# Kernel tuning notes

Measured on AMD Instinct MI355X. Metric: run time of the kernel, lower is better.

The kernel has to match this reference:

```python
import jax, jax.numpy as jnp
import numpy as np

B, S, E, H = 2, 2048, 1024, 16
D = E // H  # head_dim = 64


def setup_inputs() -> dict:
    key = jax.random.key(0)
    ks = jax.random.split(key, 6)
    scale = 1.0 / np.sqrt(E)
    x = jax.random.normal(ks[0], (B, S, E), dtype=jnp.float32)
    mask = jnp.ones((B, S), dtype=jnp.int32)
    Wqkv = jax.random.normal(ks[1], (E, 3 * E), dtype=jnp.float32) * scale
    bqkv = jax.random.normal(ks[2], (3 * E,), dtype=jnp.float32) * 0.01
    Wout = jax.random.normal(ks[3], (E, E), dtype=jnp.float32) * scale
    bout = jax.random.normal(ks[4], (E,), dtype=jnp.float32) * 0.01
    return {"x": x, "mask": mask, "Wqkv": Wqkv, "bqkv": bqkv, "Wout": Wout, "bout": bout}


def reference(x, mask, Wqkv, bqkv, Wout, bout):
    Bn, Sn, En = x.shape
    qkv = x @ Wqkv + bqkv                      # [B,S,3E]
    qkv = qkv.reshape(Bn, Sn, 3, H, D)
    qkv = jnp.transpose(qkv, (2, 0, 3, 1, 4))  # [3,B,H,S,D]
    q, k, v = qkv[0], qkv[1], qkv[2]
    scores = jnp.einsum('bhqd,bhkd->bhqk', q, k) / np.sqrt(D).astype(np.float32)
    m = mask[:, None, None, :]                 # [B,1,1,S]
    scores = jnp.where(m == 0, jnp.float32(-jnp.inf), scores)
    attn = jax.nn.softmax(scores, axis=-1)
    out = jnp.einsum('bhqk,bhkd->bhqd', attn, v)  # [B,H,S,D]
    out = jnp.transpose(out, (0, 2, 1, 3)).reshape(Bn, Sn, En)
    return out @ Wout + bout
```

## Files before the change

kernel.cpp:

```cpp
#include <hip/hip_runtime.h>


typedef __attribute__((ext_vector_type(8))) short short8;
typedef __attribute__((ext_vector_type(4))) float floatx4;
typedef unsigned short ushort_t;

static __device__ __forceinline__ ushort_t f2bf(float f) {
    unsigned u = __float_as_uint(f);
    u += 0x7fffu + ((u >> 16) & 1u);
    return (ushort_t)(u >> 16);
}
static __device__ __forceinline__ float bf2f(ushort_t h) {
    return __uint_as_float(((unsigned)h) << 16);
}
#if __has_builtin(__builtin_amdgcn_cvt_pk_bf16_f32)
typedef __attribute__((ext_vector_type(2))) __bf16 bf16x2_t;
static __device__ __forceinline__ unsigned pack2bf(float a, float b) {
    bf16x2_t r = __builtin_amdgcn_cvt_pk_bf16_f32(a, b);
    return __builtin_bit_cast(unsigned, r);
}
#else
static __device__ __forceinline__ unsigned pack2bf(float a, float b) {
    return (unsigned)f2bf(a) | ((unsigned)f2bf(b) << 16);
}
#endif
static __device__ __forceinline__ float hexp2(float x) {
    return __builtin_amdgcn_exp2f(x);
}
static __device__ __forceinline__ void gload16(const void* g, void* l) {
    __builtin_amdgcn_global_load_lds(
        (const __attribute__((address_space(1))) unsigned int*)g,
        (__attribute__((address_space(3))) unsigned int*)l, 16, 0, 0);
}

__global__ __launch_bounds__(256) void conv_hi(const float* __restrict__ in,
                                               ushort_t* __restrict__ out) {
    int i = blockIdx.x * 256 + threadIdx.x;
    float4 v = ((const float4*)in)[i];
    uint2 o;
    o.x = pack2bf(v.x, v.y);
    o.y = pack2bf(v.z, v.w);
    ((uint2*)out)[i] = o;
}

__global__ __launch_bounds__(256) void conv_T_hi(const float* __restrict__ W,
                                                 ushort_t* __restrict__ hiT,
                                                 int K, int N) {
    __shared__ float tile[32][33];
    const int nb = blockIdx.x * 32, kb = blockIdx.y * 32;
    const int t = threadIdx.x;
    const int r = t >> 3, c4 = (t & 7) * 4;
    float4 v = *(const float4*)&W[(size_t)(kb + r) * N + nb + c4];
    tile[r][c4 + 0] = v.x; tile[r][c4 + 1] = v.y;
    tile[r][c4 + 2] = v.z; tile[r][c4 + 3] = v.w;
    __syncthreads();
    uint2 o;
    o.x = pack2bf(tile[c4 + 0][r], tile[c4 + 1][r]);
    o.y = pack2bf(tile[c4 + 2][r], tile[c4 + 3][r]);
    size_t off = ((size_t)(nb + r) * K + kb + c4) >> 2;
    ((uint2*)hiT)[off] = o;
}

__global__ __launch_bounds__(256) void transpose_v(const ushort_t* __restrict__ qkvb,
                                                   ushort_t* __restrict__ vtg) {
    __shared__ ushort_t tile[64][72];
    const int b = blockIdx.z, h = blockIdx.y, s0 = blockIdx.x * 64;
    const int t = threadIdx.x;
    #pragma unroll
    for (int p = 0; p < 2; ++p) {
        int idx = t + p * 256;
        int sl = idx >> 3, dc = (idx & 7) * 8;
        *(uint4*)&tile[sl][dc] =
            *(const uint4*)&qkvb[(size_t)(b * 2048 + s0 + sl) * 3072 + 2048 + h * 64 + dc];
    }
    __syncthreads();
    #pragma unroll
    for (int p = 0; p < 2; ++p) {
        int idx = t + p * 256;
        int dl = idx >> 3, sc = (idx & 7) * 8;
        ushort_t v[8];
        #pragma unroll
        for (int j = 0; j < 8; ++j) v[j] = tile[sc + j][dl];
        *(uint4*)&vtg[(size_t)((b * 16 + h) * 64 + dl) * 2048 + s0 + sc] = *(const uint4*)v;
    }
}

__global__ __launch_bounds__(256, 3) void gemm_bf16_bf(
    const ushort_t* __restrict__ A, const ushort_t* __restrict__ B,
    const float* __restrict__ bias, ushort_t* __restrict__ C,
    int M, int N, int K)
{
    __shared__ ushort_t Ah[128][32], Bh[128][32];
    const int bn = blockIdx.x * 128, bm = blockIdx.y * 128;
    const int t = threadIdx.x, w = t >> 6, lane = t & 63;
    const int l15 = lane & 15, quad = lane >> 4;
    const int wm = w >> 1, wn = w & 1;

    const int srow = w * 32 + (lane >> 2);
    const int skp  = (lane & 3) ^ ((lane >> 2) & 3);
    const int scol = skp * 8;
    const ushort_t* ga = A + (size_t)(bm + srow) * K + scol;
    const ushort_t* gb = B + (size_t)(bn + srow) * K + scol;
    const size_t rstep = (size_t)16 * K;
    const int fcol = ((quad ^ (l15 & 3)) * 8);

    floatx4 acc[4][4];
    #pragma unroll
    for (int mt = 0; mt < 4; ++mt)
        #pragma unroll
        for (int nt = 0; nt < 4; ++nt) acc[mt][nt] = (floatx4){0.f, 0.f, 0.f, 0.f};

    for (int k0 = 0; k0 < K; k0 += 32) {
        #pragma unroll
        for (int i = 0; i < 2; ++i) {
            gload16(ga + i * rstep + k0, &Ah[w * 32 + i * 16][0]);
            gload16(gb + i * rstep + k0, &Bh[w * 32 + i * 16][0]);
        }
        __syncthreads();
        short8 ah[4], bh[4];
        #pragma unroll
        for (int x = 0; x < 4; ++x) {
            ah[x] = *(const short8*)&Ah[wm * 64 + x * 16 + l15][fcol];
            bh[x] = *(const short8*)&Bh[wn * 64 + x * 16 + l15][fcol];
        }
        #pragma unroll
        for (int mt = 0; mt < 4; ++mt)
            #pragma unroll
            for (int nt = 0; nt < 4; ++nt)
                acc[mt][nt] = __builtin_amdgcn_mfma_f32_16x16x32_bf16(ah[mt], bh[nt], acc[mt][nt], 0, 0, 0);
        __syncthreads();
    }
    #pragma unroll
    for (int mt = 0; mt < 4; ++mt)
        #pragma unroll
        for (int r = 0; r < 4; ++r) {
            size_t row = (size_t)(bm + wm * 64 + mt * 16 + quad * 4 + r) * N;
            #pragma unroll
            for (int nt = 0; nt < 4; ++nt) {
                int col = bn + wn * 64 + nt * 16 + l15;
                C[row + col] = f2bf(acc[mt][nt][r] + bias[col]);
            }
        }
}

__global__ __launch_bounds__(256, 3) void gemm_bf16_f32_64(
    const ushort_t* __restrict__ A, const ushort_t* __restrict__ B,
    const float* __restrict__ bias, float* __restrict__ C,
    int M, int N, int K)
{
    __shared__ ushort_t Ah[64][32], Bh[128][32];
    const int bn = blockIdx.x * 128, bm = blockIdx.y * 64;
    const int t = threadIdx.x, w = t >> 6, lane = t & 63;
    const int l15 = lane & 15, quad = lane >> 4;
    const int wm = w >> 1, wn = w & 1;

    const int srow = w * 16 + (lane >> 2);
    const int skp  = (lane & 3) ^ ((lane >> 2) & 3);
    const int scol = skp * 8;
    const ushort_t* ga  = A + (size_t)(bm + srow) * K + scol;
    const ushort_t* gb0 = B + (size_t)(bn + srow) * K + scol;
    const ushort_t* gb1 = B + (size_t)(bn + 64 + srow) * K + scol;
    const int fcol = ((quad ^ (l15 & 3)) * 8);

    floatx4 acc[2][4];
    #pragma unroll
    for (int mt = 0; mt < 2; ++mt)
        #pragma unroll
        for (int nt = 0; nt < 4; ++nt) acc[mt][nt] = (floatx4){0.f, 0.f, 0.f, 0.f};

    for (int k0 = 0; k0 < K; k0 += 32) {
        gload16(ga  + k0, &Ah[w * 16][0]);
        gload16(gb0 + k0, &Bh[w * 16][0]);
        gload16(gb1 + k0, &Bh[64 + w * 16][0]);
        __syncthreads();
        short8 ah[2], bh[4];
        #pragma unroll
        for (int x = 0; x < 2; ++x)
            ah[x] = *(const short8*)&Ah[wm * 32 + x * 16 + l15][fcol];
        #pragma unroll
        for (int x = 0; x < 4; ++x)
            bh[x] = *(const short8*)&Bh[wn * 64 + x * 16 + l15][fcol];
        #pragma unroll
        for (int mt = 0; mt < 2; ++mt)
            #pragma unroll
            for (int nt = 0; nt < 4; ++nt)
                acc[mt][nt] = __builtin_amdgcn_mfma_f32_16x16x32_bf16(ah[mt], bh[nt], acc[mt][nt], 0, 0, 0);
        __syncthreads();
    }
    #pragma unroll
    for (int mt = 0; mt < 2; ++mt)
        #pragma unroll
        for (int r = 0; r < 4; ++r) {
            size_t row = (size_t)(bm + wm * 32 + mt * 16 + quad * 4 + r) * N;
            #pragma unroll
            for (int nt = 0; nt < 4; ++nt) {
                int col = bn + wn * 64 + nt * 16 + l15;
                C[row + col] = acc[mt][nt][r] + bias[col];
            }
        }
}

__global__ __launch_bounds__(256, 3) void flash_v5(
    const ushort_t* __restrict__ qkv, const ushort_t* __restrict__ vtg,
    const int* __restrict__ mask,
    ushort_t* __restrict__ po0, ushort_t* __restrict__ po1,
    float* __restrict__ pl0, float* __restrict__ pl1, int S)
{
    __shared__ ushort_t Ks[64][64];
    __shared__ ushort_t Vt[64][64];
    __shared__ ushort_t Ps[4][16][72];
    __shared__ float Madd[64];

    const int blk = blockIdx.x;
    const int xcd = blk & 7, rr = blk >> 3;
    const int qi = rr & 15, g = xcd + 8 * (rr >> 4);
    const int half = g & 1, h = (g >> 1) & 15, b = g >> 5;
    const int q0 = qi * 128;
    const int kbase = half * 1024;

    ushort_t* po = half ? po1 : po0;
    float*    pl = half ? pl1 : pl0;

    const int t = threadIdx.x, wave = t >> 6, lane = t & 63;
    const int l15 = lane & 15, quad = lane >> 4;
    const size_t bS = (size_t)b * S;
    const float c1  = 0.125f * 1.44269504088896340736f;
    const float OFF = 24.0f;

    short8 qf[2][2];
    #pragma unroll
    for (int tt = 0; tt < 2; ++tt) {
        int q = q0 + wave * 32 + tt * 16 + l15;
        const ushort_t* qp = qkv + (bS + q) * 3072 + h * 64;
        qf[tt][0] = *(const short8*)(qp + quad * 8);
        qf[tt][1] = *(const short8*)(qp + 32 + quad * 8);
    }

    const int srow  = wave * 16 + (lane >> 3);
    const int schnk = ((lane & 7) ^ ((lane >> 3) & 7)) * 8;
    const ushort_t* gK = qkv + (bS + srow) * 3072 + 1024 + h * 64 + schnk;
    const ushort_t* gV = vtg + ((size_t)(b * 16 + h) * 64 + srow) * 2048 + schnk;

    floatx4 outacc[2][4];
    float lsum[2] = {0.f, 0.f};
    #pragma unroll
    for (int tt = 0; tt < 2; ++tt)
        #pragma unroll
        for (int dt = 0; dt < 4; ++dt) outacc[tt][dt] = (floatx4){0.f, 0.f, 0.f, 0.f};

    for (int k0 = kbase; k0 < kbase + 1024; k0 += 64) {
        gload16(gK + (size_t)k0 * 3072,             &Ks[wave * 16][0]);
        gload16(gK + (size_t)k0 * 3072 + 8 * 3072,  &Ks[wave * 16 + 8][0]);
        gload16(gV + k0,                            &Vt[wave * 16][0]);
        gload16(gV + k0 + 8 * 2048,                 &Vt[wave * 16 + 8][0]);
        if (t < 64) Madd[t] = (mask[bS + k0 + t] ? 0.f : -1e30f) - OFF;
        __syncthreads();

        short8 kf[2][4], vf[2][4];
        #pragma unroll
        for (int kc = 0; kc < 2; ++kc)
            #pragma unroll
            for (int c = 0; c < 4; ++c) {
                int ch = ((kc * 4 + quad) ^ (l15 & 7)) * 8;
                kf[kc][c] = *(const short8*)&Ks[c * 16 + l15][ch];
                vf[kc][c] = *(const short8*)&Vt[c * 16 + l15][ch];
            }
        float4 madd4[4];
        #pragma unroll
        for (int c = 0; c < 4; ++c) madd4[c] = *(const float4*)&Madd[c * 16 + quad * 4];

        #pragma unroll
        for (int tt = 0; tt < 2; ++tt) {
            floatx4 sc[4];
            #pragma unroll
            for (int c = 0; c < 4; ++c) {
                sc[c] = (floatx4){0.f, 0.f, 0.f, 0.f};
                sc[c] = __builtin_amdgcn_mfma_f32_16x16x32_bf16(kf[0][c], qf[tt][0], sc[c], 0, 0, 0);
                sc[c] = __builtin_amdgcn_mfma_f32_16x16x32_bf16(kf[1][c], qf[tt][1], sc[c], 0, 0, 0);
            }
            #pragma unroll
            for (int c = 0; c < 4; ++c) {
                float p0 = hexp2(fmaf(sc[c][0], c1, madd4[c].x));
                float p1 = hexp2(fmaf(sc[c][1], c1, madd4[c].y));
                float p2 = hexp2(fmaf(sc[c][2], c1, madd4[c].z));
                float p3 = hexp2(fmaf(sc[c][3], c1, madd4[c].w));
                lsum[tt] += (p0 + p1) + (p2 + p3);
                uint2 pk;
                pk.x = pack2bf(p0, p1);
                pk.y = pack2bf(p2, p3);
                *(uint2*)&Ps[wave][l15][c * 16 + quad * 4] = pk;
            }
            short8 pf0 = *(const short8*)&Ps[wave][l15][quad * 8];
            short8 pf1 = *(const short8*)&Ps[wave][l15][32 + quad * 8];
            #pragma unroll
            for (int dt = 0; dt < 4; ++dt) {
                outacc[tt][dt] = __builtin_amdgcn_mfma_f32_16x16x32_bf16(vf[0][dt], pf0, outacc[tt][dt], 0, 0, 0);
                outacc[tt][dt] = __builtin_amdgcn_mfma_f32_16x16x32_bf16(vf[1][dt], pf1, outacc[tt][dt], 0, 0, 0);
            }
        }
        __syncthreads();
    }

    #pragma unroll
    for (int tt = 0; tt < 2; ++tt) {
        lsum[tt] += __shfl_xor(lsum[tt], 16);
        lsum[tt] += __shfl_xor(lsum[tt], 32);
        lsum[tt] += 1e-30f;
        float inv = 1.f / lsum[tt];
        int q = q0 + wave * 32 + tt * 16 + l15;
        ushort_t* orow = po + (bS + q) * 1024 + h * 64;
        #pragma unroll
        for (int dt = 0; dt < 4; ++dt) {
            uint2 pk;
            pk.x = pack2bf(outacc[tt][dt][0] * inv, outacc[tt][dt][1] * inv);
            pk.y = pack2bf(outacc[tt][dt][2] * inv, outacc[tt][dt][3] * inv);
            *(uint2*)&orow[dt * 16 + quad * 4] = pk;
        }
        if (quad == 0) pl[(bS + q) * 16 + h] = lsum[tt];
    }
}

__global__ __launch_bounds__(256) void combine_halves(
    const ushort_t* __restrict__ po0, const ushort_t* __restrict__ po1,
    const float* __restrict__ pl0, const float* __restrict__ pl1,
    ushort_t* __restrict__ attnb)
{
    int i = blockIdx.x * 256 + threadIdx.x;
    int row = i >> 8;
    int h = (i >> 4) & 15;
    float l0 = pl0[row * 16 + h], l1 = pl1[row * 16 + h];
    float inv = 1.f / (l0 + l1);
    float w0 = l0 * inv, w1 = l1 * inv;
    uint2 a = ((const uint2*)po0)[i];
    uint2 b2 = ((const uint2*)po1)[i];
    float o0 = bf2f(a.x & 0xffff)  * w0 + bf2f(b2.x & 0xffff)  * w1;
    float o1 = bf2f(a.x >> 16)     * w0 + bf2f(b2.x >> 16)     * w1;
    float o2 = bf2f(a.y & 0xffff)  * w0 + bf2f(b2.y & 0xffff)  * w1;
    float o3 = bf2f(a.y >> 16)     * w0 + bf2f(b2.y >> 16)     * w1;
    uint2 o;
    o.x = pack2bf(o0, o1);
    o.y = pack2bf(o2, o3);
    ((uint2*)attnb)[i] = o;
}

extern "C" void kernel_launch(void* const* d_in, const int* in_sizes, int n_in,
                              void* d_out, int out_size, void* d_ws, size_t ws_size,
                              hipStream_t stream) {
    const float* x    = (const float*)d_in[0];
    const int*   mask = (const int*)  d_in[1];
    const float* Wqkv = (const float*)d_in[2];
    const float* bqkv = (const float*)d_in[3];
    const float* Wout = (const float*)d_in[4];
    const float* bout = (const float*)d_in[5];
    float* out = (float*)d_out;

    char* ws = (char*)d_ws;
    ushort_t* qkvb = (ushort_t*)(ws);
    ushort_t* attnb= (ushort_t*)(ws + 25165824);
    ushort_t* vtg  = (ushort_t*)(ws + 33554432);
    ushort_t* woT  = (ushort_t*)(ws + 41943040);
    ushort_t* xb   = (ushort_t*)(ws + 44040192);
    ushort_t* wqT  = (ushort_t*)(ws + 52428800);
    ushort_t* po0  = (ushort_t*)(ws + 44040192);
    ushort_t* po1  = (ushort_t*)(ws + 52428800);
    float*    pl0  = (float*)   (ws + 60817408);
    float*    pl1  = (float*)   (ws + 61079552);

    const int M = 4096, E = 1024, N3 = 3072, S = 2048;

    conv_hi<<<dim3(M * E / 1024), dim3(256), 0, stream>>>(x, xb);
    conv_T_hi<<<dim3(N3 / 32, E / 32), dim3(256), 0, stream>>>(Wqkv, wqT, E, N3);

    gemm_bf16_bf<<<dim3(N3 / 128, M / 128), dim3(256), 0, stream>>>(
        xb, wqT, bqkv, qkvb, M, N3, E);

    transpose_v<<<dim3(S / 64, 16, 2), dim3(256), 0, stream>>>(qkvb, vtg);

    flash_v5<<<dim3(1024), dim3(256), 0, stream>>>(
        qkvb, vtg, mask, po0, po1, pl0, pl1, S);

    combine_halves<<<dim3(M * E / 4 / 256), dim3(256), 0, stream>>>(
        po0, po1, pl0, pl1, attnb);

    conv_T_hi<<<dim3(E / 32, E / 32), dim3(256), 0, stream>>>(Wout, woT, E, E);

    gemm_bf16_f32_64<<<dim3(E / 128, M / 64), dim3(256), 0, stream>>>(
        attnb, woT, bout, out, M, E, E);
}
```

Before: 221.5 us.

## Fuse V transpose into QKV GEMM epilogue and drop split-K attention combine

The QKV GEMM epilogue now writes the V columns directly in transposed layout, so the separate transpose kernel is removed. Q and K are stored packed into a 2048-wide buffer. The flash kernel now processes the full key range per block (512 blocks instead of 1024), which eliminates the partial outputs and the combine_halves pass. It also double-buffers the K/V tiles in LDS, loads a precomputed additive mask once into LDS, and lowers occupancy to 2 blocks per CU. The trade-off is half as many attention blocks, a longer per-block loop, and more LDS per block.

New measurement: 208.2 us. 1.06x faster.

```diff
diff --git a/kernel.cpp b/kernel.cpp
--- a/kernel.cpp
+++ b/kernel.cpp
@@ -61,35 +61,18 @@
     ((uint2*)hiT)[off] = o;
 }
 
-__global__ __launch_bounds__(256) void transpose_v(const ushort_t* __restrict__ qkvb,
-                                                   ushort_t* __restrict__ vtg) {
-    __shared__ ushort_t tile[64][72];
-    const int b = blockIdx.z, h = blockIdx.y, s0 = blockIdx.x * 64;
-    const int t = threadIdx.x;
-    #pragma unroll
-    for (int p = 0; p < 2; ++p) {
-        int idx = t + p * 256;
-        int sl = idx >> 3, dc = (idx & 7) * 8;
-        *(uint4*)&tile[sl][dc] =
-            *(const uint4*)&qkvb[(size_t)(b * 2048 + s0 + sl) * 3072 + 2048 + h * 64 + dc];
-    }
-    __syncthreads();
-    #pragma unroll
-    for (int p = 0; p < 2; ++p) {
-        int idx = t + p * 256;
-        int dl = idx >> 3, sc = (idx & 7) * 8;
-        ushort_t v[8];
-        #pragma unroll
-        for (int j = 0; j < 8; ++j) v[j] = tile[sc + j][dl];
-        *(uint4*)&vtg[(size_t)((b * 16 + h) * 64 + dl) * 2048 + s0 + sc] = *(const uint4*)v;
-    }
-}
-
-__global__ __launch_bounds__(256, 3) void gemm_bf16_bf(
+__global__ __launch_bounds__(256) void conv_madd(const int* __restrict__ mask,
+                                                 float* __restrict__ maddg) {
+    int i = blockIdx.x * 256 + threadIdx.x;
+    maddg[i] = (mask[i] ? 0.f : -1e30f) - 24.0f;
+}
+
+__global__ __launch_bounds__(256, 3) void gemm_qkv(
     const ushort_t* __restrict__ A, const ushort_t* __restrict__ B,
-    const float* __restrict__ bias, ushort_t* __restrict__ C,
-    int M, int N, int K)
+    const float* __restrict__ bias, ushort_t* __restrict__ qkvb,
+    ushort_t* __restrict__ vtg)
 {
+    const int K = 1024;
     __shared__ ushort_t Ah[128][32], Bh[128][32];
     const int bn = blockIdx.x * 128, bm = blockIdx.y * 128;
     const int t = threadIdx.x, w = t >> 6, lane = t & 63;
@@ -130,17 +113,37 @@
                 acc[mt][nt] = __builtin_amdgcn_mfma_f32_16x16x32_bf16(ah[mt], bh[nt], acc[mt][nt], 0, 0, 0);
         __syncthreads();
     }
-    #pragma unroll
-    for (int mt = 0; mt < 4; ++mt)
-        #pragma unroll
-        for (int r = 0; r < 4; ++r) {
-            size_t row = (size_t)(bm + wm * 64 + mt * 16 + quad * 4 + r) * N;
+
+    if (bn < 2048) {
+        #pragma unroll
+        for (int mt = 0; mt < 4; ++mt)
+            #pragma unroll
+            for (int r = 0; r < 4; ++r) {
+                size_t row = (size_t)(bm + wm * 64 + mt * 16 + quad * 4 + r) * 2048;
+                #pragma unroll
+                for (int nt = 0; nt < 4; ++nt) {
+                    int col = bn + wn * 64 + nt * 16 + l15;
+                    qkvb[row + col] = f2bf(acc[mt][nt][r] + bias[col]);
+                }
+            }
+    } else {
+        const int h = (bn - 2048 + wn * 64) >> 6;
+        #pragma unroll
+        for (int mt = 0; mt < 4; ++mt) {
+            int brow = bm + wm * 64 + mt * 16 + quad * 4;
+            int b = brow >> 11, s = brow & 2047;
             #pragma unroll
             for (int nt = 0; nt < 4; ++nt) {
                 int col = bn + wn * 64 + nt * 16 + l15;
-                C[row + col] = f2bf(acc[mt][nt][r] + bias[col]);
-            }
-        }
+                int d = nt * 16 + l15;
+                float bv = bias[col];
+                uint2 pk;
+                pk.x = pack2bf(acc[mt][nt][0] + bv, acc[mt][nt][1] + bv);
+                pk.y = pack2bf(acc[mt][nt][2] + bv, acc[mt][nt][3] + bv);
+                *(uint2*)&vtg[((size_t)((b * 16 + h) * 64 + d)) * 2048 + s] = pk;
+            }
+        }
+    }
 }
 
 __global__ __launch_bounds__(256, 3) void gemm_bf16_f32_64(
@@ -200,46 +203,49 @@
         }
 }
 
-__global__ __launch_bounds__(256, 3) void flash_v5(
+__global__ __launch_bounds__(256, 2) void flash_v6(
     const ushort_t* __restrict__ qkv, const ushort_t* __restrict__ vtg,
-    const int* __restrict__ mask,
-    ushort_t* __restrict__ po0, ushort_t* __restrict__ po1,
-    float* __restrict__ pl0, float* __restrict__ pl1, int S)
+    const float* __restrict__ maddg, ushort_t* __restrict__ attn)
 {
-    __shared__ ushort_t Ks[64][64];
-    __shared__ ushort_t Vt[64][64];
-    __shared__ ushort_t Ps[4][16][72];
-    __shared__ float Madd[64];
+    __shared__ ushort_t Ks[2][64][64];
+    __shared__ ushort_t Vt[2][64][64];
+    __shared__ ushort_t Ps[4][2][16][72];
+    __shared__ float MaddL[2048];
 
     const int blk = blockIdx.x;
     const int xcd = blk & 7, rr = blk >> 3;
     const int qi = rr & 15, g = xcd + 8 * (rr >> 4);
-    const int half = g & 1, h = (g >> 1) & 15, b = g >> 5;
-    const int q0 = qi * 128;
-    const int kbase = half * 1024;
-
-    ushort_t* po = half ? po1 : po0;
-    float*    pl = half ? pl1 : pl0;
+    const int b = g >> 4, h = g & 15, q0 = qi * 128;
 
     const int t = threadIdx.x, wave = t >> 6, lane = t & 63;
     const int l15 = lane & 15, quad = lane >> 4;
-    const size_t bS = (size_t)b * S;
-    const float c1  = 0.125f * 1.44269504088896340736f;
-    const float OFF = 24.0f;
+    const size_t bS = (size_t)b * 2048;
+    const float c1 = 0.125f * 1.44269504088896340736f;
 
     short8 qf[2][2];
     #pragma unroll
     for (int tt = 0; tt < 2; ++tt) {
         int q = q0 + wave * 32 + tt * 16 + l15;
-        const ushort_t* qp = qkv + (bS + q) * 3072 + h * 64;
+        const ushort_t* qp = qkv + (bS + q) * 2048 + h * 64;
         qf[tt][0] = *(const short8*)(qp + quad * 8);
         qf[tt][1] = *(const short8*)(qp + 32 + quad * 8);
     }
 
     const int srow  = wave * 16 + (lane >> 3);
     const int schnk = ((lane & 7) ^ ((lane >> 3) & 7)) * 8;
-    const ushort_t* gK = qkv + (bS + srow) * 3072 + 1024 + h * 64 + schnk;
+    const ushort_t* gK = qkv + (bS + srow) * 2048 + 1024 + h * 64 + schnk;
     const ushort_t* gV = vtg + ((size_t)(b * 16 + h) * 64 + srow) * 2048 + schnk;
+
+    gload16(gK,            &Ks[0][wave * 16][0]);
+    gload16(gK + 8 * 2048, &Ks[0][wave * 16 + 8][0]);
+    gload16(gV,            &Vt[0][wave * 16][0]);
+    gload16(gV + 8 * 2048, &Vt[0][wave * 16 + 8][0]);
+    {
+        const float* gM = maddg + b * 2048 + wave * 512 + lane * 4;
+        gload16(gM,       &MaddL[wave * 512]);
+        gload16(gM + 256, &MaddL[wave * 512 + 256]);
+    }
+    __syncthreads();
 
     floatx4 outacc[2][4];
     float lsum[2] = {0.f, 0.f};
@@ -248,13 +254,17 @@
         #pragma unroll
         for (int dt = 0; dt < 4; ++dt) outacc[tt][dt] = (floatx4){0.f, 0.f, 0.f, 0.f};
 
-    for (int k0 = kbase; k0 < kbase + 1024; k0 += 64) {
-        gload16(gK + (size_t)k0 * 3072,             &Ks[wave * 16][0]);
-        gload16(gK + (size_t)k0 * 3072 + 8 * 3072,  &Ks[wave * 16 + 8][0]);
-        gload16(gV + k0,                            &Vt[wave * 16][0]);
-        gload16(gV + k0 + 8 * 2048,                 &Vt[wave * 16 + 8][0]);
-        if (t < 64) Madd[t] = (mask[bS + k0 + t] ? 0.f : -1e30f) - OFF;
-        __syncthreads();
+    int cur = 0;
+    for (int kt = 0; kt < 32; ++kt) {
+        const int k0 = kt * 64;
+        {
+            const int kn = (kt + 1 < 32) ? (kt + 1) * 64 : 0;
+            const int nb = cur ^ 1;
+            gload16(gK + (size_t)kn * 2048,            &Ks[nb][wave * 16][0]);
+            gload16(gK + (size_t)(kn + 8) * 2048,      &Ks[nb][wave * 16 + 8][0]);
+            gload16(gV + kn,                           &Vt[nb][wave * 16][0]);
+            gload16(gV + kn + 8 * 2048,                &Vt[nb][wave * 16 + 8][0]);
+        }
 
         short8 kf[2][4], vf[2][4];
         #pragma unroll
@@ -262,12 +272,13 @@
             #pragma unroll
             for (int c = 0; c < 4; ++c) {
                 int ch = ((kc * 4 + quad) ^ (l15 & 7)) * 8;
-                kf[kc][c] = *(const short8*)&Ks[c * 16 + l15][ch];
-                vf[kc][c] = *(const short8*)&Vt[c * 16 + l15][ch];
+                kf[kc][c] = *(const short8*)&Ks[cur][c * 16 + l15][ch];
+                vf[kc][c] = *(const short8*)&Vt[cur][c * 16 + l15][ch];
             }
         float4 madd4[4];
         #pragma unroll
-        for (int c = 0; c < 4; ++c) madd4[c] = *(const float4*)&Madd[c * 16 + quad * 4];
+        for (int c = 0; c < 4; ++c)
+            madd4[c] = *(const float4*)&MaddL[k0 + c * 16 + quad * 4];
 
         #pragma unroll
         for (int tt = 0; tt < 2; ++tt) {
@@ -288,10 +299,10 @@
                 uint2 pk;
                 pk.x = pack2bf(p0, p1);
                 pk.y = pack2bf(p2, p3);
-                *(uint2*)&Ps[wave][l15][c * 16 + quad * 4] = pk;
-            }
-            short8 pf0 = *(const short8*)&Ps[wave][l15][quad * 8];
-            short8 pf1 = *(const short8*)&Ps[wave][l15][32 + quad * 8];
+                *(uint2*)&Ps[wave][tt][l15][c * 16 + quad * 4] = pk;
+            }
+            short8 pf0 = *(const short8*)&Ps[wave][tt][l15][quad * 8];
+            short8 pf1 = *(const short8*)&Ps[wave][tt][l15][32 + quad * 8];
             #pragma unroll
             for (int dt = 0; dt < 4; ++dt) {
                 outacc[tt][dt] = __builtin_amdgcn_mfma_f32_16x16x32_bf16(vf[0][dt], pf0, outacc[tt][dt], 0, 0, 0);
@@ -299,16 +310,16 @@
             }
         }
         __syncthreads();
+        cur ^= 1;
     }
 
     #pragma unroll
     for (int tt = 0; tt < 2; ++tt) {
         lsum[tt] += __shfl_xor(lsum[tt], 16);
         lsum[tt] += __shfl_xor(lsum[tt], 32);
-        lsum[tt] += 1e-30f;
         float inv = 1.f / lsum[tt];
         int q = q0 + wave * 32 + tt * 16 + l15;
-        ushort_t* orow = po + (bS + q) * 1024 + h * 64;
+        ushort_t* orow = attn + (bS + q) * 1024 + h * 64;
         #pragma unroll
         for (int dt = 0; dt < 4; ++dt) {
             uint2 pk;
@@ -316,31 +327,7 @@
             pk.y = pack2bf(outacc[tt][dt][2] * inv, outacc[tt][dt][3] * inv);
             *(uint2*)&orow[dt * 16 + quad * 4] = pk;
         }
-        if (quad == 0) pl[(bS + q) * 16 + h] = lsum[tt];
-    }
-}
-
-__global__ __launch_bounds__(256) void combine_halves(
-    const ushort_t* __restrict__ po0, const ushort_t* __restrict__ po1,
-    const float* __restrict__ pl0, const float* __restrict__ pl1,
-    ushort_t* __restrict__ attnb)
-{
-    int i = blockIdx.x * 256 + threadIdx.x;
-    int row = i >> 8;
-    int h = (i >> 4) & 15;
-    float l0 = pl0[row * 16 + h], l1 = pl1[row * 16 + h];
-    float inv = 1.f / (l0 + l1);
-    float w0 = l0 * inv, w1 = l1 * inv;
-    uint2 a = ((const uint2*)po0)[i];
-    uint2 b2 = ((const uint2*)po1)[i];
-    float o0 = bf2f(a.x & 0xffff)  * w0 + bf2f(b2.x & 0xffff)  * w1;
-    float o1 = bf2f(a.x >> 16)     * w0 + bf2f(b2.x >> 16)     * w1;
-    float o2 = bf2f(a.y & 0xffff)  * w0 + bf2f(b2.y & 0xffff)  * w1;
-    float o3 = bf2f(a.y >> 16)     * w0 + bf2f(b2.y >> 16)     * w1;
-    uint2 o;
-    o.x = pack2bf(o0, o1);
-    o.y = pack2bf(o2, o3);
-    ((uint2*)attnb)[i] = o;
+    }
 }
 
 extern "C" void kernel_launch(void* const* d_in, const int* in_sizes, int n_in,
@@ -355,32 +342,24 @@
     float* out = (float*)d_out;
 
     char* ws = (char*)d_ws;
-    ushort_t* qkvb = (ushort_t*)(ws);
-    ushort_t* attnb= (ushort_t*)(ws + 25165824);
-    ushort_t* vtg  = (ushort_t*)(ws + 33554432);
-    ushort_t* woT  = (ushort_t*)(ws + 41943040);
-    ushort_t* xb   = (ushort_t*)(ws + 44040192);
-    ushort_t* wqT  = (ushort_t*)(ws + 52428800);
-    ushort_t* po0  = (ushort_t*)(ws + 44040192);
-    ushort_t* po1  = (ushort_t*)(ws + 52428800);
-    float*    pl0  = (float*)   (ws + 60817408);
-    float*    pl1  = (float*)   (ws + 61079552);
+    ushort_t* xb    = (ushort_t*)(ws);
+    ushort_t* wqT   = (ushort_t*)(ws + 8388608);
+    ushort_t* qkvb  = (ushort_t*)(ws + 14680064);
+    ushort_t* vtg   = (ushort_t*)(ws + 31457280);
+    ushort_t* attnb = (ushort_t*)(ws + 39845888);
+    ushort_t* woT   = (ushort_t*)(ws + 48234496);
+    float*    maddg = (float*)   (ws + 50331648);
 
     const int M = 4096, E = 1024, N3 = 3072, S = 2048;
 
     conv_hi<<<dim3(M * E / 1024), dim3(256), 0, stream>>>(x, xb);
     conv_T_hi<<<dim3(N3 / 32, E / 32), dim3(256), 0, stream>>>(Wqkv, wqT, E, N3);
-
-    gemm_bf16_bf<<<dim3(N3 / 128, M / 128), dim3(256), 0, stream>>>(
-        xb, wqT, bqkv, qkvb, M, N3, E);
-
-    transpose_v<<<dim3(S / 64, 16, 2), dim3(256), 0, stream>>>(qkvb, vtg);
-
-    flash_v5<<<dim3(1024), dim3(256), 0, stream>>>(
-        qkvb, vtg, mask, po0, po1, pl0, pl1, S);
-
-    combine_halves<<<dim3(M * E / 4 / 256), dim3(256), 0, stream>>>(
-        po0, po1, pl0, pl1, attnb);
+    conv_madd<<<dim3(M / 256), dim3(256), 0, stream>>>(mask, maddg);
+
+    gemm_qkv<<<dim3(N3 / 128, M / 128), dim3(256), 0, stream>>>(
+        xb, wqT, bqkv, qkvb, vtg);
+
+    flash_v6<<<dim3(512), dim3(256), 0, stream>>>(qkvb, vtg, maddg, attnb);
 
     conv_T_hi<<<dim3(E / 32, E / 32), dim3(256), 0, stream>>>(Wout, woT, E, E);
 
```
